# Kernel tuning notes

Measured on AMD Instinct MI355X. Metric: run time of the kernel, lower is better.

Reference implementation:

```python
import jax, jax.numpy as jnp
import numpy as np

D_MODEL = 768
D_HEAD = 64
BATCH = 2
SEQ = 4096


def setup_inputs() -> dict:
    key = jax.random.key(0)
    k1, k2, k3, k4, k5 = jax.random.split(key, 5)
    x = jax.random.normal(k1, (BATCH, SEQ, D_MODEL), dtype=jnp.float32)
    # causal mask as the module expects: (seq_len, seq_len) float, 1 where attend allowed
    mask = jnp.tril(jnp.ones((SEQ, SEQ), dtype=jnp.float32))
    # weights initialized like the module: randn / sqrt(d_model)
    scale = 1.0 / np.sqrt(D_MODEL)
    Wq = jax.random.normal(k2, (D_HEAD, D_MODEL), dtype=jnp.float32) * scale
    Wk = jax.random.normal(k3, (D_HEAD, D_MODEL), dtype=jnp.float32) * scale
    Wv = jax.random.normal(k4, (D_HEAD, D_MODEL), dtype=jnp.float32) * scale
    Wo = jax.random.normal(k5, (D_MODEL, D_HEAD), dtype=jnp.float32) * scale
    return {"x": x, "mask": mask, "Wq": Wq, "Wk": Wk, "Wv": Wv, "Wo": Wo}


def reference(x, mask, Wq, Wk, Wv, Wo):
    # q,k,v: (B, S, d_head); Linear with weight (out,in) => x @ W.T
    q = jnp.einsum('bsm,hm->bsh', x, Wq)
    k = jnp.einsum('bsm,hm->bsh', x, Wk)
    v = jnp.einsum('bsm,hm->bsh', x, Wv)
    scores = jnp.einsum('bqd,bkd->bqk', q, k) / np.sqrt(D_HEAD)  # (B,S,S)
    seq_len = x.shape[1]
    m = mask[:seq_len, :seq_len]
    # faithful to the torch code: tril(scores) - 1e10 * (1 - mask)
    scores = jnp.tril(scores) - 1e10 * (1.0 - m)
    attn = jax.nn.softmax(scores, axis=-1)
    z = jnp.einsum('bqk,bkd->bqd', attn, v)  # (B,S,d_head)
    out = jnp.einsum('bsh,mh->bsm', z, Wo)   # (B,S,d_model)
    return out
```

## Files before the change

### kernel.cpp

```cpp
#include <hip/hip_runtime.h>
#include <stdint.h>

#define SEQ 4096
#define DM 768
#define DH 64

typedef __attribute__((ext_vector_type(8))) short short8;
typedef __attribute__((ext_vector_type(4))) short short4v;
typedef __attribute__((ext_vector_type(4))) float f32x4;

#define LOG2E 1.4426950408889634f

static __device__ __forceinline__ short bf16r(float f) {
  union { float f; uint32_t u; } v; v.f = f;
  uint32_t u = v.u;
  return (short)((u + 0x7FFFu + ((u >> 16) & 1u)) >> 16);
}

static __device__ __forceinline__ float bf16f(uint16_t u) {
  union { uint32_t u; float f; } v; v.u = ((uint32_t)u) << 16;
  return v.f;
}

static __device__ __forceinline__ int swz(int row, int b) {
  return row * 128 + (b ^ ((row & 7) << 4));
}

__global__ __launch_bounds__(256) void convert_w(
    const float* __restrict__ Wq, const float* __restrict__ Wk,
    const float* __restrict__ Wv, const float* __restrict__ Wo,
    uint16_t* __restrict__ Wb, uint16_t* __restrict__ Wob) {
  int id = blockIdx.x * 256 + threadIdx.x;
  if (id < 36864) {
    int row = id / 192, c4 = id % 192;
    const float* src = (row < 64) ? (Wq + (size_t)row * DM)
                     : (row < 128) ? (Wk + (size_t)(row - 64) * DM)
                                   : (Wv + (size_t)(row - 128) * DM);
    const float sc = (row < 64) ? (0.125f * LOG2E) : 1.0f;
    float4 v = *(const float4*)(src + c4 * 4);
    short4v pk = { bf16r(v.x * sc), bf16r(v.y * sc), bf16r(v.z * sc), bf16r(v.w * sc) };
    *(short4v*)(Wb + (size_t)row * DM + c4 * 4) = pk;
  } else {
    int t = id - 36864;
    int row = t >> 4, c4 = t & 15;
    float4 v = *(const float4*)(Wo + (size_t)row * DH + c4 * 4);
    short4v pk = { bf16r(v.x), bf16r(v.y), bf16r(v.z), bf16r(v.w) };
    *(short4v*)(Wob + (size_t)row * DH + c4 * 4) = pk;
  }
}

__global__ __launch_bounds__(256) void qkv_proj(
    const float* __restrict__ x, const uint16_t* __restrict__ Wb,
    uint16_t* __restrict__ qg, uint16_t* __restrict__ kg, uint16_t* __restrict__ vg) {
  __shared__ char smem[2048 + 24576] __attribute__((aligned(16)));
  char* Xl = smem;
  char* Wl = smem + 2048;
  const int tid = threadIdx.x;
  const int lane = tid & 63, wv = tid >> 6;
  const int l15 = lane & 15, l4 = lane >> 4;
  const int row0 = blockIdx.x * 16;

  const int xr = tid >> 4, xc4 = tid & 15;
  const int wr0 = tid >> 3, wb16 = tid & 7;

  f32x4 acc[3];
  #pragma unroll
  for (int j = 0; j < 3; ++j) acc[j] = (f32x4){0.f, 0.f, 0.f, 0.f};

  float4 xreg;
  short8 wreg[6];
  xreg = *(const float4*)(x + (size_t)(row0 + xr) * DM + xc4 * 4);
  #pragma unroll
  for (int i = 0; i < 6; ++i)
    wreg[i] = *(const short8*)(Wb + (size_t)(wr0 + i * 32) * DM + wb16 * 8);

  for (int t = 0; t < 12; ++t) {
    __syncthreads();
    {
      short4v pk = { bf16r(xreg.x), bf16r(xreg.y), bf16r(xreg.z), bf16r(xreg.w) };
      *(short4v*)(Xl + swz(xr, xc4 * 8)) = pk;
    }
    #pragma unroll
    for (int i = 0; i < 6; ++i)
      *(short8*)(Wl + swz(wr0 + i * 32, wb16 * 16)) = wreg[i];
    __syncthreads();
    if (t < 11) {
      const int k0n = (t + 1) * 64;
      xreg = *(const float4*)(x + (size_t)(row0 + xr) * DM + k0n + xc4 * 4);
      #pragma unroll
      for (int i = 0; i < 6; ++i)
        wreg[i] = *(const short8*)(Wb + (size_t)(wr0 + i * 32) * DM + k0n + wb16 * 8);
    }
    #pragma unroll
    for (int kc = 0; kc < 2; ++kc) {
      short8 af = *(const short8*)(Xl + swz(l15, kc * 64 + l4 * 16));
      #pragma unroll
      for (int j = 0; j < 3; ++j) {
        int nt = wv * 3 + j;
        short8 bfv = *(const short8*)(Wl + swz(nt * 16 + l15, kc * 64 + l4 * 16));
        acc[j] = __builtin_amdgcn_mfma_f32_16x16x32_bf16(af, bfv, acc[j], 0, 0, 0);
      }
    }
  }
  #pragma unroll
  for (int j = 0; j < 3; ++j) {
    int nt = wv * 3 + j;
    uint16_t* dst = (nt < 4) ? qg : (nt < 8) ? kg : vg;
    int cb = (nt & 3) * 16 + l15;
    #pragma unroll
    for (int r = 0; r < 4; ++r) {
      int row = row0 + l4 * 4 + r;
      dst[(size_t)row * DH + cb] = (uint16_t)bf16r(acc[j][r]);
    }
  }
}

__global__ __launch_bounds__(256) void attn_split(
    const uint16_t* __restrict__ qg, const uint16_t* __restrict__ kg,
    const uint16_t* __restrict__ vg, uint16_t* __restrict__ zg,
    uint16_t* __restrict__ Opart, float* __restrict__ Ml, int CHUNK, int MAXCH) {
  __shared__ char smem[8192 * 2 + 4 * 2048] __attribute__((aligned(16)));
  char* Kl = smem;
  char* Vl = smem + 8192;
  char* Pl = smem + 16384;

  const int tid = threadIdx.x;
  const int lane = tid & 63, wv = tid >> 6;
  const int l15 = lane & 15, l4 = lane >> 4;
  const int qt = blockIdx.x, ch = blockIdx.y, b = blockIdx.z;
  const int q0 = qt << 6;
  const int kv_lim = q0 + 64;
  const int kv_begin = ch * CHUNK;
  if (kv_begin >= kv_lim) return;
  const int kv_end = min(kv_begin + CHUNK, kv_lim);
  const int ntiles = (kv_end - kv_begin) >> 6;

  const uint16_t* qb = qg + (size_t)b * SEQ * DH;
  const uint16_t* kb = kg + (size_t)b * SEQ * DH;
  const uint16_t* vb = vg + (size_t)b * SEQ * DH;

  const int qrow = q0 + wv * 16 + l15;
  short8 qf0 = *(const short8*)(qb + (size_t)qrow * DH + l4 * 8);
  short8 qf1 = *(const short8*)(qb + (size_t)qrow * DH + 32 + l4 * 8);

  const int ku = tid - 128;
  const int vg_ = tid >> 3, vdg = tid & 7;
  short8 sreg[4];

  {
    const int kv0 = kv_begin;
    if (tid >= 128) {
      #pragma unroll
      for (int i = 0; i < 4; ++i) {
        int c = ku + (i << 7);
        sreg[i] = *(const short8*)(kb + (size_t)(kv0 + (c >> 3)) * DH + (c & 7) * 8);
      }
    } else {
      #pragma unroll
      for (int i = 0; i < 4; ++i)
        sreg[i] = *(const short8*)(vb + (size_t)(kv0 + vg_ * 4 + i) * DH + vdg * 8);
    }
  }

  f32x4 oaccT[4];
  #pragma unroll
  for (int n = 0; n < 4; ++n) oaccT[n] = (f32x4){0.f, 0.f, 0.f, 0.f};
  float lrun = 0.f;

  for (int T = 0; T < ntiles; ++T) {
    const int kv0 = kv_begin + (T << 6);
    __syncthreads();
    if (tid >= 128) {
      #pragma unroll
      for (int i = 0; i < 4; ++i) {
        int c = ku + (i << 7);
        *(short8*)(Kl + swz(c >> 3, (c & 7) * 16)) = sreg[i];
      }
    } else {
      #pragma unroll
      for (int j = 0; j < 8; ++j) {
        int d = vdg * 8 + j;
        short4v pk = { sreg[0][j], sreg[1][j], sreg[2][j], sreg[3][j] };
        *(short4v*)(Vl + d * 128 + ((vg_ * 8) ^ ((d & 7) << 4))) = pk;
      }
    }
    __syncthreads();
    if (T + 1 < ntiles) {
      const int kvn = kv0 + 64;
      if (tid >= 128) {
        #pragma unroll
        for (int i = 0; i < 4; ++i) {
          int c = ku + (i << 7);
          sreg[i] = *(const short8*)(kb + (size_t)(kvn + (c >> 3)) * DH + (c & 7) * 8);
        }
      } else {
        #pragma unroll
        for (int i = 0; i < 4; ++i)
          sreg[i] = *(const short8*)(vb + (size_t)(kvn + vg_ * 4 + i) * DH + vdg * 8);
      }
    }

    f32x4 sacc[4];
    #pragma unroll
    for (int n = 0; n < 4; ++n) sacc[n] = (f32x4){0.f, 0.f, 0.f, 0.f};
    #pragma unroll
    for (int n = 0; n < 4; ++n) {
      short8 kf0 = *(const short8*)(Kl + swz(n * 16 + l15, l4 * 16));
      sacc[n] = __builtin_amdgcn_mfma_f32_16x16x32_bf16(kf0, qf0, sacc[n], 0, 0, 0);
      short8 kf1 = *(const short8*)(Kl + swz(n * 16 + l15, 64 + l4 * 16));
      sacc[n] = __builtin_amdgcn_mfma_f32_16x16x32_bf16(kf1, qf1, sacc[n], 0, 0, 0);
    }

    if (kv0 + 63 > q0) {
      #pragma unroll
      for (int n = 0; n < 4; ++n) {
        #pragma unroll
        for (int r = 0; r < 4; ++r) {
          int kvg = kv0 + n * 16 + l4 * 4 + r;
          if (kvg > qrow) sacc[n][r] = -1e30f;
        }
      }
    }

    float ls = 0.f;
    #pragma unroll
    for (int n = 0; n < 4; ++n) {
      #pragma unroll
      for (int r = 0; r < 4; ++r) {
        float p = exp2f(sacc[n][r]);
        sacc[n][r] = p;
        ls += p;
      }
    }
    ls += __shfl_xor(ls, 16);
    ls += __shfl_xor(ls, 32);
    lrun += ls;

    char* Pw = Pl + wv * 2048;
    #pragma unroll
    for (int n = 0; n < 4; ++n) {
      short4v pk = { bf16r(sacc[n][0]), bf16r(sacc[n][1]),
                     bf16r(sacc[n][2]), bf16r(sacc[n][3]) };
      *(short4v*)(Pw + swz(l15, n * 32 + l4 * 8)) = pk;
    }
    asm volatile("s_waitcnt lgkmcnt(0)" ::: "memory");
    short8 pa0 = *(const short8*)(Pw + swz(l15, l4 * 16));
    short8 pa1 = *(const short8*)(Pw + swz(l15, 64 + l4 * 16));
    #pragma unroll
    for (int n = 0; n < 4; ++n) {
      int dr = n * 16 + l15;
      short8 vf0 = *(const short8*)(Vl + dr * 128 + ((l4 * 16) ^ ((dr & 7) << 4)));
      oaccT[n] = __builtin_amdgcn_mfma_f32_16x16x32_bf16(vf0, pa0, oaccT[n], 0, 0, 0);
      short8 vf1 = *(const short8*)(Vl + dr * 128 + ((64 + l4 * 16) ^ ((dr & 7) << 4)));
      oaccT[n] = __builtin_amdgcn_mfma_f32_16x16x32_bf16(vf1, pa1, oaccT[n], 0, 0, 0);
    }
  }

  const int rl = wv * 16 + l15;
  if (MAXCH == 1) {
    float invl = 1.0f / lrun;
    uint16_t* zb = zg + (size_t)b * SEQ * DH;
    #pragma unroll
    for (int n = 0; n < 4; ++n) {
      short4v pk = { bf16r(oaccT[n][0] * invl), bf16r(oaccT[n][1] * invl),
                     bf16r(oaccT[n][2] * invl), bf16r(oaccT[n][3] * invl) };
      *(short4v*)(zb + (size_t)(q0 + rl) * DH + n * 16 + l4 * 4) = pk;
    }
  } else {
    const size_t slot = ((size_t)(b << 6) + qt) * MAXCH + ch;
    uint16_t* op = Opart + slot * 4096;
    #pragma unroll
    for (int n = 0; n < 4; ++n) {
      short4v pk = { bf16r(oaccT[n][0]), bf16r(oaccT[n][1]),
                     bf16r(oaccT[n][2]), bf16r(oaccT[n][3]) };
      *(short4v*)(op + (size_t)rl * 64 + n * 16 + l4 * 4) = pk;
    }
    if (l4 == 0) Ml[slot * 64 + rl] = lrun;
  }
}

__global__ __launch_bounds__(256) void out_proj(
    const uint16_t* __restrict__ Opart, const float* __restrict__ Ml,
    const uint16_t* __restrict__ zg, const uint16_t* __restrict__ Wob,
    float* __restrict__ out, int CHUNK, int MAXCH) {
  __shared__ char smem[4096 + 32768] __attribute__((aligned(16)));
  char* Zl = smem;
  char* Wl = smem + 4096;
  const int tid = threadIdx.x;
  const int lane = tid & 63, wv = tid >> 6;
  const int l15 = lane & 15, l4 = lane >> 4;
  const int row0 = blockIdx.x * 32;
  const int col0 = blockIdx.y * 256;

  {
    const int r = tid >> 3, c0 = (tid & 7) << 3;
    if (MAXCH == 1) {
      short8 v = *(const short8*)(zg + (size_t)(row0 + r) * DH + c0);
      *(short8*)(Zl + swz(r, c0 * 2)) = v;
    } else {
      const int b = row0 >> 12;
      const int rlb = row0 & 4095;
      const int qt = rlb >> 6, q0 = qt << 6;
      const int row_local = (rlb & 63) + r;
      const int nch = (q0 + 64 + CHUNK - 1) / CHUNK;
      const size_t sbase = ((size_t)(b << 6) + qt) * MAXCH;
      float a[8] = {0.f, 0.f, 0.f, 0.f, 0.f, 0.f, 0.f, 0.f};
      float wsum = 0.f;
      for (int ch = 0; ch < nch; ++ch) {
        const size_t s = sbase + ch;
        wsum += Ml[s * 64 + row_local];
        short8 v = *(const short8*)(Opart + s * 4096 + (size_t)row_local * 64 + c0);
        #pragma unroll
        for (int j = 0; j < 8; ++j) a[j] += bf16f((uint16_t)v[j]);
      }
      float inv = 1.0f / wsum;
      short8 pk;
      #pragma unroll
      for (int j = 0; j < 8; ++j) pk[j] = bf16r(a[j] * inv);
      *(short8*)(Zl + swz(r, c0 * 2)) = pk;
    }
  }
  #pragma unroll
  for (int i = 0; i < 8; ++i) {
    int id = tid + (i << 8);
    int m = id >> 3, c8 = id & 7;
    short8 vw = *(const short8*)(Wob + (size_t)(col0 + m) * DH + c8 * 8);
    *(short8*)(Wl + swz(m, c8 * 16)) = vw;
  }
  __syncthreads();

  const int mh = wv & 1, ng = wv >> 1;
  short8 af0 = *(const short8*)(Zl + swz(mh * 16 + l15, l4 * 16));
  short8 af1 = *(const short8*)(Zl + swz(mh * 16 + l15, 64 + l4 * 16));
  f32x4 acc[8];
  #pragma unroll
  for (int j = 0; j < 8; ++j) acc[j] = (f32x4){0.f, 0.f, 0.f, 0.f};
  #pragma unroll
  for (int j = 0; j < 8; ++j) {
    int nt = ng * 8 + j;
    short8 b0 = *(const short8*)(Wl + swz(nt * 16 + l15, l4 * 16));
    acc[j] = __builtin_amdgcn_mfma_f32_16x16x32_bf16(af0, b0, acc[j], 0, 0, 0);
    short8 b1 = *(const short8*)(Wl + swz(nt * 16 + l15, 64 + l4 * 16));
    acc[j] = __builtin_amdgcn_mfma_f32_16x16x32_bf16(af1, b1, acc[j], 0, 0, 0);
  }
  #pragma unroll
  for (int j = 0; j < 8; ++j) {
    int nt = ng * 8 + j;
    #pragma unroll
    for (int r = 0; r < 4; ++r) {
      int row = row0 + mh * 16 + l4 * 4 + r;
      int col = col0 + nt * 16 + l15;
      out[(size_t)row * DM + col] = acc[j][r];
    }
  }
}

extern "C" void kernel_launch(void* const* d_in, const int* in_sizes, int n_in,
                              void* d_out, int out_size, void* d_ws, size_t ws_size,
                              hipStream_t stream) {
  const float* x  = (const float*)d_in[0];
  const float* Wq = (const float*)d_in[2];
  const float* Wk = (const float*)d_in[3];
  const float* Wv = (const float*)d_in[4];
  const float* Wo = (const float*)d_in[5];
  float* out = (float*)d_out;

  const size_t N = (size_t)2 * SEQ * DH;
  uint16_t* qg = (uint16_t*)d_ws;
  uint16_t* kg = qg + N;
  uint16_t* vg = kg + N;
  uint16_t* zg = vg + N;
  uint16_t* Wb = zg + N;
  const size_t WBE = (size_t)192 * DM;
  uint16_t* Wob = Wb + WBE;
  const size_t WOE = (size_t)DM * DH;
  uint16_t* Opart = Wob + WOE;

  int maxch = 16;
  while (maxch > 1) {
    size_t slots = (size_t)2 * 64 * maxch;
    size_t need = 4 * N * 2 + WBE * 2 + WOE * 2 + slots * (4096 * 2 + 64 * 4);
    if (need <= ws_size) break;
    maxch >>= 1;
  }
  const int CHUNK = SEQ / maxch;
  float* Ml = (float*)(Opart + (size_t)2 * 64 * maxch * 4096);

  convert_w<<<192, 256, 0, stream>>>(Wq, Wk, Wv, Wo, Wb, Wob);
  qkv_proj<<<512, 256, 0, stream>>>(x, Wb, qg, kg, vg);
  attn_split<<<dim3(64, maxch, 2), 256, 0, stream>>>(qg, kg, vg, zg, Opart, Ml,
                                                     CHUNK, maxch);
  out_proj<<<dim3(256, 3), 256, 0, stream>>>(Opart, Ml, zg, Wob, out, CHUNK, maxch);
}
```

Before: 53.39 us.

## Double-buffer K/V tiles in attention and widen QKV projection row tiles

```diff
diff --git a/kernel.cpp b/kernel.cpp
--- a/kernel.cpp
+++ b/kernel.cpp
@@ -52,24 +52,26 @@
 __global__ __launch_bounds__(256) void qkv_proj(
     const float* __restrict__ x, const uint16_t* __restrict__ Wb,
     uint16_t* __restrict__ qg, uint16_t* __restrict__ kg, uint16_t* __restrict__ vg) {
-  __shared__ char smem[2048 + 24576] __attribute__((aligned(16)));
+  __shared__ char smem[4096 + 24576] __attribute__((aligned(16)));
   char* Xl = smem;
-  char* Wl = smem + 2048;
+  char* Wl = smem + 4096;
   const int tid = threadIdx.x;
   const int lane = tid & 63, wv = tid >> 6;
   const int l15 = lane & 15, l4 = lane >> 4;
-  const int row0 = blockIdx.x * 16;
+  const int row0 = blockIdx.x * 32;
 
   const int xr = tid >> 4, xc4 = tid & 15;
   const int wr0 = tid >> 3, wb16 = tid & 7;
-
-  f32x4 acc[3];
-  #pragma unroll
-  for (int j = 0; j < 3; ++j) acc[j] = (f32x4){0.f, 0.f, 0.f, 0.f};
-
-  float4 xreg;
+  const int mh = wv & 1, ng = wv >> 1;
+
+  f32x4 acc[6];
+  #pragma unroll
+  for (int j = 0; j < 6; ++j) acc[j] = (f32x4){0.f, 0.f, 0.f, 0.f};
+
+  float4 xreg[2];
   short8 wreg[6];
-  xreg = *(const float4*)(x + (size_t)(row0 + xr) * DM + xc4 * 4);
+  xreg[0] = *(const float4*)(x + (size_t)(row0 + xr) * DM + xc4 * 4);
+  xreg[1] = *(const float4*)(x + (size_t)(row0 + 16 + xr) * DM + xc4 * 4);
   #pragma unroll
   for (int i = 0; i < 6; ++i)
     wreg[i] = *(const short8*)(Wb + (size_t)(wr0 + i * 32) * DM + wb16 * 8);
@@ -77,8 +79,10 @@
   for (int t = 0; t < 12; ++t) {
     __syncthreads();
     {
-      short4v pk = { bf16r(xreg.x), bf16r(xreg.y), bf16r(xreg.z), bf16r(xreg.w) };
-      *(short4v*)(Xl + swz(xr, xc4 * 8)) = pk;
+      short4v p0 = { bf16r(xreg[0].x), bf16r(xreg[0].y), bf16r(xreg[0].z), bf16r(xreg[0].w) };
+      *(short4v*)(Xl + swz(xr, xc4 * 8)) = p0;
+      short4v p1 = { bf16r(xreg[1].x), bf16r(xreg[1].y), bf16r(xreg[1].z), bf16r(xreg[1].w) };
+      *(short4v*)(Xl + swz(xr + 16, xc4 * 8)) = p1;
     }
     #pragma unroll
     for (int i = 0; i < 6; ++i)
@@ -86,30 +90,31 @@
     __syncthreads();
     if (t < 11) {
       const int k0n = (t + 1) * 64;
-      xreg = *(const float4*)(x + (size_t)(row0 + xr) * DM + k0n + xc4 * 4);
+      xreg[0] = *(const float4*)(x + (size_t)(row0 + xr) * DM + k0n + xc4 * 4);
+      xreg[1] = *(const float4*)(x + (size_t)(row0 + 16 + xr) * DM + k0n + xc4 * 4);
       #pragma unroll
       for (int i = 0; i < 6; ++i)
         wreg[i] = *(const short8*)(Wb + (size_t)(wr0 + i * 32) * DM + k0n + wb16 * 8);
     }
     #pragma unroll
     for (int kc = 0; kc < 2; ++kc) {
-      short8 af = *(const short8*)(Xl + swz(l15, kc * 64 + l4 * 16));
-      #pragma unroll
-      for (int j = 0; j < 3; ++j) {
-        int nt = wv * 3 + j;
+      short8 af = *(const short8*)(Xl + swz(mh * 16 + l15, kc * 64 + l4 * 16));
+      #pragma unroll
+      for (int j = 0; j < 6; ++j) {
+        int nt = ng * 6 + j;
         short8 bfv = *(const short8*)(Wl + swz(nt * 16 + l15, kc * 64 + l4 * 16));
         acc[j] = __builtin_amdgcn_mfma_f32_16x16x32_bf16(af, bfv, acc[j], 0, 0, 0);
       }
     }
   }
   #pragma unroll
-  for (int j = 0; j < 3; ++j) {
-    int nt = wv * 3 + j;
+  for (int j = 0; j < 6; ++j) {
+    int nt = ng * 6 + j;
     uint16_t* dst = (nt < 4) ? qg : (nt < 8) ? kg : vg;
     int cb = (nt & 3) * 16 + l15;
     #pragma unroll
     for (int r = 0; r < 4; ++r) {
-      int row = row0 + l4 * 4 + r;
+      int row = row0 + mh * 16 + l4 * 4 + r;
       dst[(size_t)row * DH + cb] = (uint16_t)bf16r(acc[j][r]);
     }
   }
@@ -119,10 +124,8 @@
     const uint16_t* __restrict__ qg, const uint16_t* __restrict__ kg,
     const uint16_t* __restrict__ vg, uint16_t* __restrict__ zg,
     uint16_t* __restrict__ Opart, float* __restrict__ Ml, int CHUNK, int MAXCH) {
-  __shared__ char smem[8192 * 2 + 4 * 2048] __attribute__((aligned(16)));
-  char* Kl = smem;
-  char* Vl = smem + 8192;
-  char* Pl = smem + 16384;
+  __shared__ char smem[32768 + 4 * 2048] __attribute__((aligned(16)));
+  char* Pl = smem + 32768;
 
   const int tid = threadIdx.x;
   const int lane = tid & 63, wv = tid >> 6;
@@ -147,20 +150,41 @@
   const int vg_ = tid >> 3, vdg = tid & 7;
   short8 sreg[4];
 
-  {
-    const int kv0 = kv_begin;
-    if (tid >= 128) {
-      #pragma unroll
-      for (int i = 0; i < 4; ++i) {
-        int c = ku + (i << 7);
-        sreg[i] = *(const short8*)(kb + (size_t)(kv0 + (c >> 3)) * DH + (c & 7) * 8);
-      }
-    } else {
-      #pragma unroll
-      for (int i = 0; i < 4; ++i)
-        sreg[i] = *(const short8*)(vb + (size_t)(kv0 + vg_ * 4 + i) * DH + vdg * 8);
-    }
-  }
+#define LOAD_REGS(KV0)                                                              \
+  if (tid >= 128) {                                                                 \
+    _Pragma("unroll")                                                               \
+    for (int i = 0; i < 4; ++i) {                                                   \
+      int c = ku + (i << 7);                                                        \
+      sreg[i] = *(const short8*)(kb + (size_t)((KV0) + (c >> 3)) * DH + (c & 7) * 8); \
+    }                                                                               \
+  } else {                                                                          \
+    _Pragma("unroll")                                                               \
+    for (int i = 0; i < 4; ++i)                                                     \
+      sreg[i] = *(const short8*)(vb + (size_t)((KV0) + vg_ * 4 + i) * DH + vdg * 8); \
+  }
+
+#define STAGE_WRITE(BUF)                                                            \
+  {                                                                                 \
+    char* Kl_ = smem + (BUF) * 16384;                                               \
+    char* Vl_ = smem + (BUF) * 16384 + 8192;                                        \
+    if (tid >= 128) {                                                               \
+      _Pragma("unroll")                                                             \
+      for (int i = 0; i < 4; ++i) {                                                 \
+        int c = ku + (i << 7);                                                      \
+        *(short8*)(Kl_ + swz(c >> 3, (c & 7) * 16)) = sreg[i];                      \
+      }                                                                             \
+    } else {                                                                        \
+      _Pragma("unroll")                                                             \
+      for (int j = 0; j < 8; ++j) {                                                 \
+        int d = vdg * 8 + j;                                                        \
+        short4v pk = { sreg[0][j], sreg[1][j], sreg[2][j], sreg[3][j] };            \
+        *(short4v*)(Vl_ + d * 128 + ((vg_ * 8) ^ ((d & 7) << 4))) = pk;             \
+      }                                                                             \
+    }                                                                               \
+  }
+
+  LOAD_REGS(kv_begin);
+  STAGE_WRITE(0);
 
   f32x4 oaccT[4];
   #pragma unroll
@@ -169,36 +193,11 @@
 
   for (int T = 0; T < ntiles; ++T) {
     const int kv0 = kv_begin + (T << 6);
+    if (T + 1 < ntiles) { LOAD_REGS(kv0 + 64); }
     __syncthreads();
-    if (tid >= 128) {
-      #pragma unroll
-      for (int i = 0; i < 4; ++i) {
-        int c = ku + (i << 7);
-        *(short8*)(Kl + swz(c >> 3, (c & 7) * 16)) = sreg[i];
-      }
-    } else {
-      #pragma unroll
-      for (int j = 0; j < 8; ++j) {
-        int d = vdg * 8 + j;
-        short4v pk = { sreg[0][j], sreg[1][j], sreg[2][j], sreg[3][j] };
-        *(short4v*)(Vl + d * 128 + ((vg_ * 8) ^ ((d & 7) << 4))) = pk;
-      }
-    }
-    __syncthreads();
-    if (T + 1 < ntiles) {
-      const int kvn = kv0 + 64;
-      if (tid >= 128) {
-        #pragma unroll
-        for (int i = 0; i < 4; ++i) {
-          int c = ku + (i << 7);
-          sreg[i] = *(const short8*)(kb + (size_t)(kvn + (c >> 3)) * DH + (c & 7) * 8);
-        }
-      } else {
-        #pragma unroll
-        for (int i = 0; i < 4; ++i)
-          sreg[i] = *(const short8*)(vb + (size_t)(kvn + vg_ * 4 + i) * DH + vdg * 8);
-      }
-    }
+    const int cur = T & 1;
+    char* Kl = smem + cur * 16384;
+    char* Vl = smem + cur * 16384 + 8192;
 
     f32x4 sacc[4];
     #pragma unroll
@@ -254,7 +253,11 @@
       short8 vf1 = *(const short8*)(Vl + dr * 128 + ((64 + l4 * 16) ^ ((dr & 7) << 4)));
       oaccT[n] = __builtin_amdgcn_mfma_f32_16x16x32_bf16(vf1, pa1, oaccT[n], 0, 0, 0);
     }
-  }
+
+    if (T + 1 < ntiles) { STAGE_WRITE((T + 1) & 1); }
+  }
+#undef LOAD_REGS
+#undef STAGE_WRITE
 
   const int rl = wv * 16 + l15;
   if (MAXCH == 1) {
@@ -387,7 +390,7 @@
   float* Ml = (float*)(Opart + (size_t)2 * 64 * maxch * 4096);
 
   convert_w<<<192, 256, 0, stream>>>(Wq, Wk, Wv, Wo, Wb, Wob);
-  qkv_proj<<<512, 256, 0, stream>>>(x, Wb, qg, kg, vg);
+  qkv_proj<<<256, 256, 0, stream>>>(x, Wb, qg, kg, vg);
   attn_split<<<dim3(64, maxch, 2), 256, 0, stream>>>(qg, kg, vg, zg, Opart, Ml,
                                                      CHUNK, maxch);
   out_proj<<<dim3(256, 3), 256, 0, stream>>>(Opart, Ml, zg, Wob, out, CHUNK, maxch);
```

New measurement: 53.69 us. No clear change (+0.6%).
